# Optimization experiments

Measured on AMD Instinct MI355X. Metric: run time of the kernel, lower is better.

The kernel has to match this reference:

```python
import jax, jax.numpy as jnp
import numpy as np

B, S, D = 2, 2048, 1024
H, DH = 16, 64
EPS = 1e-5

def setup_inputs() -> dict:
    key = jax.random.key(0)
    ks = jax.random.split(key, 8)
    s = 0.02
    return {
        "x": jax.random.normal(ks[0], (B, S, D), dtype=jnp.float32),
        "ln_gamma": jnp.ones((D,), jnp.float32),
        "ln_beta": jnp.zeros((D,), jnp.float32),
        "wq": jax.random.normal(ks[1], (D, H * DH), jnp.float32) * s,
        "bq": jnp.zeros((H * DH,), jnp.float32),
        "wk": jax.random.normal(ks[2], (D, H * DH), jnp.float32) * s,
        "bk": jnp.zeros((H * DH,), jnp.float32),
        "wv": jax.random.normal(ks[3], (D, H * DH), jnp.float32) * s,
        "bv": jnp.zeros((H * DH,), jnp.float32),
        "wo": jax.random.normal(ks[4], (H * DH, D), jnp.float32) * s,
        "bo": jnp.zeros((D,), jnp.float32),
    }

def reference(x, ln_gamma, ln_beta, wq, bq, wk, bk, wv, bv, wo, bo):
    # Pre-LayerNorm over d_model
    mu = jnp.mean(x, axis=-1, keepdims=True)
    var = jnp.var(x, axis=-1, keepdims=True)
    xn = (x - mu) * jax.lax.rsqrt(var + EPS) * ln_gamma + ln_beta

    b, s, _ = xn.shape
    q = (xn @ wq + bq).reshape(b, s, H, DH)
    k = (xn @ wk + bk).reshape(b, s, H, DH)
    v = (xn @ wv + bv).reshape(b, s, H, DH)

    scale = jnp.sqrt(jnp.float32(DH))
    scores = jnp.einsum('bihd,bjhd->bhij', q, k) / scale  # [b,h,s,s]
    att = jax.nn.softmax(scores, axis=-1)
    out = jnp.einsum('bhij,bjhd->bihd', att, v).reshape(b, s, H * DH)
    return out @ wo + bo
```

## Files before the change

kernel.cpp:

```cpp
#include <hip/hip_runtime.h>
#include <math.h>

#define SEQ   2048
#define DM    1024
#define NHEAD 16
#define HD    64
#define NTOK  4096
#define EPS   1e-5f
#define SCALE_C 0.18033688f

typedef __attribute__((ext_vector_type(8))) short v8s;
typedef __attribute__((ext_vector_type(4))) float v4f;
typedef unsigned short ushort_t;

#define GLOAD16(g, l) __builtin_amdgcn_global_load_lds( \
    (const __attribute__((address_space(1))) unsigned int*)(g), \
    (__attribute__((address_space(3))) unsigned int*)(l), 16, 0, 0)

__device__ __forceinline__ unsigned short f2bf(float f) {
  union { float f; unsigned u; } v; v.f = f;
  unsigned r = v.u + 0x7FFFu + ((v.u >> 16) & 1u);
  return (unsigned short)(r >> 16);
}

__device__ __forceinline__ unsigned pack2_bf16(float a, float b) {
  union { float f; unsigned u; } ua, ub;
  ua.f = a; ub.f = b;
  return __builtin_amdgcn_perm(ub.u + 0x8000u, ua.u + 0x8000u, 0x07060302u);
}

__global__ __launch_bounds__(256) void ln_kernel(
    const float* __restrict__ x, const float* __restrict__ g,
    const float* __restrict__ be, ushort_t* __restrict__ y) {
  const int row = blockIdx.x;
  const int t = threadIdx.x;
  const float4 v = ((const float4*)(x + (size_t)row * DM))[t];
  float s  = v.x + v.y + v.z + v.w;
  float ss = v.x*v.x + v.y*v.y + v.z*v.z + v.w*v.w;
  #pragma unroll
  for (int off = 32; off > 0; off >>= 1) {
    s  += __shfl_down(s,  off, 64);
    ss += __shfl_down(ss, off, 64);
  }
  __shared__ float red[8];
  __shared__ float mu_s, rs_s;
  const int wid = t >> 6, lane = t & 63;
  if (lane == 0) { red[wid] = s; red[4 + wid] = ss; }
  __syncthreads();
  if (t == 0) {
    const float S  = red[0] + red[1] + red[2] + red[3];
    const float SS = red[4] + red[5] + red[6] + red[7];
    const float mu  = S * (1.0f / DM);
    const float var = SS * (1.0f / DM) - mu * mu;
    mu_s = mu; rs_s = rsqrtf(var + EPS);
  }
  __syncthreads();
  const float mu = mu_s, r = rs_s;
  const float4 gv = ((const float4*)g)[t];
  const float4 bv = ((const float4*)be)[t];
  ushort4 o;
  o.x = f2bf((v.x - mu) * r * gv.x + bv.x);
  o.y = f2bf((v.y - mu) * r * gv.y + bv.y);
  o.z = f2bf((v.z - mu) * r * gv.z + bv.z);
  o.w = f2bf((v.w - mu) * r * gv.w + bv.w);
  *(ushort4*)(y + (size_t)row * DM + t * 4) = o;
}

__global__ __launch_bounds__(256) void wt_kernel(
    const float* __restrict__ w0, const float* __restrict__ w1,
    const float* __restrict__ w2, const float* __restrict__ w3,
    ushort_t* __restrict__ o0, ushort_t* __restrict__ o1,
    ushort_t* __restrict__ o2, ushort_t* __restrict__ o3) {
  const int z = blockIdx.z;
  const float* w = (z==0) ? w0 : (z==1) ? w1 : (z==2) ? w2 : w3;
  ushort_t* o    = (z==0) ? o0 : (z==1) ? o1 : (z==2) ? o2 : o3;
  __shared__ float tile[64][65];
  const int t = threadIdx.x;
  const int n0 = blockIdx.x * 64, k0 = blockIdx.y * 64;
  const int r = t >> 4, c4 = (t & 15) * 4;
  #pragma unroll
  for (int i = 0; i < 4; ++i) {
    const float4 v = *(const float4*)(w + (size_t)(k0 + r + i*16) * DM + n0 + c4);
    tile[r + i*16][c4 + 0] = v.x;
    tile[r + i*16][c4 + 1] = v.y;
    tile[r + i*16][c4 + 2] = v.z;
    tile[r + i*16][c4 + 3] = v.w;
  }
  __syncthreads();
  #pragma unroll
  for (int i = 0; i < 4; ++i) {
    const int n = r + i*16;
    ushort4 o4;
    o4.x = f2bf(tile[c4 + 0][n]);
    o4.y = f2bf(tile[c4 + 1][n]);
    o4.z = f2bf(tile[c4 + 2][n]);
    o4.w = f2bf(tile[c4 + 3][n]);
    *(ushort4*)(o + (size_t)(n0 + n) * DM + k0 + c4) = o4;
  }
}

__device__ __forceinline__ void gemm_main(ushort_t* lsa, ushort_t* lsb,
    const ushort_t* A, const ushort_t* WT, int m0, int n0, v4f acc[4][4]) {
  const int tid = threadIdx.x;
  const int wid = tid >> 6, lane = tid & 63;
  const int mh = (wid & 1) << 6, nh = (wid >> 1) << 6;
  const int r16 = lane & 15, quad = lane >> 4;
  const int srow = lane >> 2, sch = lane & 3;
  for (int k0 = 0; k0 < DM; k0 += 32) {
    __syncthreads();
    #pragma unroll
    for (int j = 0; j < 2; ++j) {
      const int o = wid * 2 + j;
      GLOAD16(A  + (size_t)(m0 + o*16 + srow) * DM + k0 + sch*8, lsa + o*512);
      GLOAD16(WT + (size_t)(n0 + o*16 + srow) * DM + k0 + sch*8, lsb + o*512);
    }
    __syncthreads();
    v8s af[4], bfr[4];
    #pragma unroll
    for (int i = 0; i < 4; ++i) {
      af[i]  = *(const v8s*)(lsa + (mh + i*16 + r16)*32 + quad*8);
      bfr[i] = *(const v8s*)(lsb + (nh + i*16 + r16)*32 + quad*8);
    }
    #pragma unroll
    for (int i = 0; i < 4; ++i)
      #pragma unroll
      for (int j = 0; j < 4; ++j)
        acc[i][j] = __builtin_amdgcn_mfma_f32_16x16x32_bf16(af[i], bfr[j], acc[i][j], 0, 0, 0);
  }
}

__global__ __launch_bounds__(256, 2) void gemm_qkv(const ushort_t* __restrict__ xn,
    const ushort_t* __restrict__ wtq, const ushort_t* __restrict__ wtk, const ushort_t* __restrict__ wtv,
    const float* __restrict__ bq, const float* __restrict__ bk, const float* __restrict__ bv,
    ushort_t* __restrict__ qo, ushort_t* __restrict__ ko, ushort_t* __restrict__ vto) {
  __shared__ ushort_t lsa[128*32];
  __shared__ ushort_t lsb[128*32];
  const int z = blockIdx.z;
  const ushort_t* WT = (z == 0) ? wtq : (z == 1) ? wtk : wtv;
  const float* bias  = (z == 0) ? bq  : (z == 1) ? bk  : bv;
  const int m0 = blockIdx.y * 128, n0 = blockIdx.x * 128;
  v4f acc[4][4];
  #pragma unroll
  for (int i = 0; i < 4; ++i)
    #pragma unroll
    for (int j = 0; j < 4; ++j) acc[i][j] = (v4f){0.f, 0.f, 0.f, 0.f};
  gemm_main(lsa, lsb, xn, WT, m0, n0, acc);
  const int tid = threadIdx.x, wid = tid >> 6, lane = tid & 63;
  const int mh = (wid & 1) << 6, nh = (wid >> 1) << 6;
  const int r16 = lane & 15, quad = lane >> 4;
  if (z < 2) {
    ushort_t* out = (z == 0) ? qo : ko;
    const float sc = (z == 0) ? SCALE_C : 1.0f;
    #pragma unroll
    for (int bn = 0; bn < 4; ++bn) {
      const int col = n0 + nh + bn*16 + r16;
      const float bb = bias[col];
      #pragma unroll
      for (int am = 0; am < 4; ++am) {
        const int tb = m0 + mh + am*16 + quad*4;
        #pragma unroll
        for (int r = 0; r < 4; ++r)
          out[(size_t)(tb + r) * DM + col] = f2bf((acc[am][bn][r] + bb) * sc);
      }
    }
  } else {
    #pragma unroll
    for (int bn = 0; bn < 4; ++bn) {
      const int col = n0 + nh + bn*16 + r16;
      const float bb = bias[col];
      const int h = col >> 6, d = col & 63;
      #pragma unroll
      for (int am = 0; am < 4; ++am) {
        const int tb = m0 + mh + am*16 + quad*4;
        const int b = tb >> 11, t = tb & 2047;
        ushort4 o4;
        o4.x = f2bf(acc[am][bn][0] + bb);
        o4.y = f2bf(acc[am][bn][1] + bb);
        o4.z = f2bf(acc[am][bn][2] + bb);
        o4.w = f2bf(acc[am][bn][3] + bb);
        *(ushort4*)(vto + ((size_t)(b*NHEAD + h) * HD + d) * SEQ + t) = o4;
      }
    }
  }
}

__global__ __launch_bounds__(256, 2) void gemm_out(const ushort_t* __restrict__ A,
    const ushort_t* __restrict__ WT, const float* __restrict__ bias,
    float* __restrict__ out) {
  __shared__ ushort_t lsa[128*32];
  __shared__ ushort_t lsb[128*32];
  const int m0 = blockIdx.y * 128, n0 = blockIdx.x * 128;
  v4f acc[4][4];
  #pragma unroll
  for (int i = 0; i < 4; ++i)
    #pragma unroll
    for (int j = 0; j < 4; ++j) acc[i][j] = (v4f){0.f, 0.f, 0.f, 0.f};
  gemm_main(lsa, lsb, A, WT, m0, n0, acc);
  const int tid = threadIdx.x, wid = tid >> 6, lane = tid & 63;
  const int mh = (wid & 1) << 6, nh = (wid >> 1) << 6;
  const int r16 = lane & 15, quad = lane >> 4;
  #pragma unroll
  for (int bn = 0; bn < 4; ++bn) {
    const int col = n0 + nh + bn*16 + r16;
    const float bb = bias[col];
    #pragma unroll
    for (int am = 0; am < 4; ++am) {
      const int tb = m0 + mh + am*16 + quad*4;
      #pragma unroll
      for (int r = 0; r < 4; ++r)
        out[(size_t)(tb + r) * DM + col] = acc[am][bn][r] + bb;
    }
  }
}

#define PROW 72
__global__ __launch_bounds__(256, 4) void attn_kernel(
    const ushort_t* __restrict__ Q, const ushort_t* __restrict__ K,
    const ushort_t* __restrict__ Vt, ushort_t* __restrict__ O) {
  __shared__ ushort_t kbuf[8*512];
  __shared__ ushort_t vbuf[8*512];
  __shared__ ushort_t ptb[4*16*PROW];
  const int tid = threadIdx.x, wid = tid >> 6, lane = tid & 63;
  const int r16 = lane & 15, quad = lane >> 4;
  const int q0 = blockIdx.x * 64, bh = blockIdx.y;
  const int b = bh >> 4, h = bh & 15;
  const ushort_t* gQ = Q + (size_t)b * SEQ * DM + h * HD;
  const ushort_t* gK = K + (size_t)b * SEQ * DM + h * HD;
  const ushort_t* gV = Vt + (size_t)bh * HD * SEQ;

  const int qtok = q0 + wid * 16 + r16;
  const v8s qf0 = *(const v8s*)(gQ + (size_t)qtok * DM + quad * 8);
  const v8s qf1 = *(const v8s*)(gQ + (size_t)qtok * DM + 32 + quad * 8);
  v4f acco[4];
  #pragma unroll
  for (int i = 0; i < 4; ++i) acco[i] = (v4f){0.f, 0.f, 0.f, 0.f};
  float lrun = 0.f;
  ushort_t* ptw = ptb + wid * 16 * PROW;

  for (int kt = 0; kt < SEQ / 64; ++kt) {
    const int k0 = kt * 64;
    __syncthreads();
    if (wid < 2) {
      #pragma unroll
      for (int j = 0; j < 4; ++j) {
        const int o = (wid & 1) * 4 + j;
        GLOAD16(gK + (size_t)(k0 + (o >> 1) * 16 + r16) * DM + (o & 1) * 32 + quad * 8,
                kbuf + o * 512);
      }
    } else {
      #pragma unroll
      for (int j = 0; j < 4; ++j) {
        const int o = (wid & 1) * 4 + j;
        GLOAD16(gV + (size_t)((o & 3) * 16 + r16) * SEQ + k0 + (o >> 2) * 32 + quad * 8,
                vbuf + o * 512);
      }
    }
    __syncthreads();

    v4f sacc[4];
    #pragma unroll
    for (int g = 0; g < 4; ++g) sacc[g] = (v4f){0.f, 0.f, 0.f, 0.f};
    #pragma unroll
    for (int g = 0; g < 4; ++g) {
      const v8s ka0 = *(const v8s*)(kbuf + (g*2 + 0) * 512 + lane * 8);
      const v8s ka1 = *(const v8s*)(kbuf + (g*2 + 1) * 512 + lane * 8);
      sacc[g] = __builtin_amdgcn_mfma_f32_16x16x32_bf16(ka0, qf0, sacc[g], 0, 0, 0);
      sacc[g] = __builtin_amdgcn_mfma_f32_16x16x32_bf16(ka1, qf1, sacc[g], 0, 0, 0);
    }

    float ls = 0.f;
    #pragma unroll
    for (int g = 0; g < 4; ++g)
      #pragma unroll
      for (int r = 0; r < 4; ++r) {
        const float e = __builtin_amdgcn_exp2f(sacc[g][r]);
        sacc[g][r] = e;
        ls += e;
      }
    ls += __shfl_xor(ls, 16, 64);
    ls += __shfl_xor(ls, 32, 64);
    lrun += ls;

    #pragma unroll
    for (int g = 0; g < 4; ++g) {
      uint2 d2;
      d2.x = pack2_bf16(sacc[g][0], sacc[g][1]);
      d2.y = pack2_bf16(sacc[g][2], sacc[g][3]);
      *(uint2*)(ptw + r16 * PROW + g*16 + quad*4) = d2;
    }

    #pragma unroll
    for (int kb = 0; kb < 2; ++kb) {
      const v8s pb = *(const v8s*)(ptw + r16 * PROW + kb*32 + quad*8);
      #pragma unroll
      for (int dg = 0; dg < 4; ++dg) {
        const v8s vf = *(const v8s*)(vbuf + (kb*4 + dg) * 512 + lane * 8);
        acco[dg] = __builtin_amdgcn_mfma_f32_16x16x32_bf16(vf, pb, acco[dg], 0, 0, 0);
      }
    }
  }

  const float inv = 1.f / lrun;
  ushort_t* gO = O + (size_t)b * SEQ * DM + h * HD;
  #pragma unroll
  for (int dg = 0; dg < 4; ++dg) {
    ushort4 o4;
    o4.x = f2bf(acco[dg][0] * inv);
    o4.y = f2bf(acco[dg][1] * inv);
    o4.z = f2bf(acco[dg][2] * inv);
    o4.w = f2bf(acco[dg][3] * inv);
    *(ushort4*)(gO + (size_t)qtok * DM + dg*16 + quad*4) = o4;
  }
}

extern "C" void kernel_launch(void* const* d_in, const int* in_sizes, int n_in,
                              void* d_out, int out_size, void* d_ws, size_t ws_size,
                              hipStream_t stream) {
  const float* x     = (const float*)d_in[0];
  const float* gamma = (const float*)d_in[1];
  const float* beta  = (const float*)d_in[2];
  const float* wq    = (const float*)d_in[3];
  const float* bq    = (const float*)d_in[4];
  const float* wk    = (const float*)d_in[5];
  const float* bk    = (const float*)d_in[6];
  const float* wv    = (const float*)d_in[7];
  const float* bv    = (const float*)d_in[8];
  const float* wo    = (const float*)d_in[9];
  const float* bo    = (const float*)d_in[10];
  float* out = (float*)d_out;

  unsigned char* w8 = (unsigned char*)d_ws;
  const size_t MB = 1024 * 1024;
  ushort_t* xn  = (ushort_t*)(w8 + 0 * MB);
  ushort_t* qb  = (ushort_t*)(w8 + 8 * MB);
  ushort_t* kb  = (ushort_t*)(w8 + 16 * MB);
  ushort_t* vt  = (ushort_t*)(w8 + 24 * MB);
  ushort_t* wtq = (ushort_t*)(w8 + 32 * MB);
  ushort_t* wtk = (ushort_t*)(w8 + 34 * MB);
  ushort_t* wtv = (ushort_t*)(w8 + 36 * MB);
  ushort_t* wto = (ushort_t*)(w8 + 38 * MB);
  ushort_t* ob  = xn;

  ln_kernel<<<dim3(NTOK), dim3(256), 0, stream>>>(x, gamma, beta, xn);
  wt_kernel<<<dim3(16, 16, 4), dim3(256), 0, stream>>>(wq, wk, wv, wo, wtq, wtk, wtv, wto);
  gemm_qkv<<<dim3(8, 32, 3), dim3(256), 0, stream>>>(xn, wtq, wtk, wtv, bq, bk, bv, qb, kb, vt);
  attn_kernel<<<dim3(SEQ / 64, 2 * NHEAD), dim3(256), 0, stream>>>(qb, kb, vt, ob);
  gemm_out<<<dim3(8, 32, 1), dim3(256), 0, stream>>>(ob, wto, bo, out);
}
```

Baseline: 214.6 us.

## Repartition attention work by key/dim per wave and shrink output GEMM tiles

The attention kernel now has each wave own a 16-key slice of the tile for all 64 queries, writing P into a shared block buffer, and a 16-wide head-dim slice for the PV product. Row sums are reduced across waves through shared memory at the end. This lets each wave load only its own K and V fragments, at the cost of an extra block barrier per key tile. Separately, the output projection switches to its own 128x64 tile loop with twice as many blocks, trading per-block reuse for more parallelism in a small GEMM.

```diff
diff --git a/kernel.cpp b/kernel.cpp
--- a/kernel.cpp
+++ b/kernel.cpp
@@ -188,19 +188,43 @@
     const ushort_t* __restrict__ WT, const float* __restrict__ bias,
     float* __restrict__ out) {
   __shared__ ushort_t lsa[128*32];
-  __shared__ ushort_t lsb[128*32];
-  const int m0 = blockIdx.y * 128, n0 = blockIdx.x * 128;
-  v4f acc[4][4];
+  __shared__ ushort_t lsb[64*32];
+  const int tid = threadIdx.x, wid = tid >> 6, lane = tid & 63;
+  const int mh = (wid & 1) * 64, nh = (wid >> 1) * 32;
+  const int r16 = lane & 15, quad = lane >> 4;
+  const int srow = lane >> 2, sch = lane & 3;
+  const int m0 = blockIdx.y * 128, n0 = blockIdx.x * 64;
+  v4f acc[4][2];
   #pragma unroll
   for (int i = 0; i < 4; ++i)
     #pragma unroll
-    for (int j = 0; j < 4; ++j) acc[i][j] = (v4f){0.f, 0.f, 0.f, 0.f};
-  gemm_main(lsa, lsb, A, WT, m0, n0, acc);
-  const int tid = threadIdx.x, wid = tid >> 6, lane = tid & 63;
-  const int mh = (wid & 1) << 6, nh = (wid >> 1) << 6;
-  const int r16 = lane & 15, quad = lane >> 4;
-  #pragma unroll
-  for (int bn = 0; bn < 4; ++bn) {
+    for (int j = 0; j < 2; ++j) acc[i][j] = (v4f){0.f, 0.f, 0.f, 0.f};
+  for (int k0 = 0; k0 < DM; k0 += 32) {
+    __syncthreads();
+    #pragma unroll
+    for (int j = 0; j < 3; ++j) {
+      const int o = wid * 3 + j;
+      if (o < 8)
+        GLOAD16(A  + (size_t)(m0 + o*16 + srow) * DM + k0 + sch*8, lsa + o*512);
+      else
+        GLOAD16(WT + (size_t)(n0 + (o-8)*16 + srow) * DM + k0 + sch*8, lsb + (o-8)*512);
+    }
+    __syncthreads();
+    v8s af[4], bfr[2];
+    #pragma unroll
+    for (int i = 0; i < 4; ++i)
+      af[i] = *(const v8s*)(lsa + (mh + i*16 + r16)*32 + quad*8);
+    #pragma unroll
+    for (int j = 0; j < 2; ++j)
+      bfr[j] = *(const v8s*)(lsb + (nh + j*16 + r16)*32 + quad*8);
+    #pragma unroll
+    for (int i = 0; i < 4; ++i)
+      #pragma unroll
+      for (int j = 0; j < 2; ++j)
+        acc[i][j] = __builtin_amdgcn_mfma_f32_16x16x32_bf16(af[i], bfr[j], acc[i][j], 0, 0, 0);
+  }
+  #pragma unroll
+  for (int bn = 0; bn < 2; ++bn) {
     const int col = n0 + nh + bn*16 + r16;
     const float bb = bias[col];
     #pragma unroll
@@ -219,7 +243,8 @@
     const ushort_t* __restrict__ Vt, ushort_t* __restrict__ O) {
   __shared__ ushort_t kbuf[8*512];
   __shared__ ushort_t vbuf[8*512];
-  __shared__ ushort_t ptb[4*16*PROW];
+  __shared__ ushort_t pbuf[64*PROW];
+  __shared__ float    lred[4][64];
   const int tid = threadIdx.x, wid = tid >> 6, lane = tid & 63;
   const int r16 = lane & 15, quad = lane >> 4;
   const int q0 = blockIdx.x * 64, bh = blockIdx.y;
@@ -228,14 +253,17 @@
   const ushort_t* gK = K + (size_t)b * SEQ * DM + h * HD;
   const ushort_t* gV = Vt + (size_t)bh * HD * SEQ;
 
-  const int qtok = q0 + wid * 16 + r16;
-  const v8s qf0 = *(const v8s*)(gQ + (size_t)qtok * DM + quad * 8);
-  const v8s qf1 = *(const v8s*)(gQ + (size_t)qtok * DM + 32 + quad * 8);
+  v8s qfr[4][2];
+  #pragma unroll
+  for (int qa = 0; qa < 4; ++qa) {
+    const ushort_t* p = gQ + (size_t)(q0 + qa*16 + r16) * DM + quad * 8;
+    qfr[qa][0] = *(const v8s*)p;
+    qfr[qa][1] = *(const v8s*)(p + 32);
+  }
   v4f acco[4];
   #pragma unroll
   for (int i = 0; i < 4; ++i) acco[i] = (v4f){0.f, 0.f, 0.f, 0.f};
-  float lrun = 0.f;
-  ushort_t* ptw = ptb + wid * 16 * PROW;
+  float lrun[4] = {0.f, 0.f, 0.f, 0.f};
 
   for (int kt = 0; kt < SEQ / 64; ++kt) {
     const int k0 = kt * 64;
@@ -257,59 +285,61 @@
     }
     __syncthreads();
 
+    const v8s ka0 = *(const v8s*)(kbuf + (wid*2 + 0) * 512 + lane * 8);
+    const v8s ka1 = *(const v8s*)(kbuf + (wid*2 + 1) * 512 + lane * 8);
     v4f sacc[4];
     #pragma unroll
-    for (int g = 0; g < 4; ++g) sacc[g] = (v4f){0.f, 0.f, 0.f, 0.f};
-    #pragma unroll
-    for (int g = 0; g < 4; ++g) {
-      const v8s ka0 = *(const v8s*)(kbuf + (g*2 + 0) * 512 + lane * 8);
-      const v8s ka1 = *(const v8s*)(kbuf + (g*2 + 1) * 512 + lane * 8);
-      sacc[g] = __builtin_amdgcn_mfma_f32_16x16x32_bf16(ka0, qf0, sacc[g], 0, 0, 0);
-      sacc[g] = __builtin_amdgcn_mfma_f32_16x16x32_bf16(ka1, qf1, sacc[g], 0, 0, 0);
-    }
-
-    float ls = 0.f;
-    #pragma unroll
-    for (int g = 0; g < 4; ++g)
-      #pragma unroll
-      for (int r = 0; r < 4; ++r) {
-        const float e = __builtin_amdgcn_exp2f(sacc[g][r]);
-        sacc[g][r] = e;
-        ls += e;
-      }
-    ls += __shfl_xor(ls, 16, 64);
-    ls += __shfl_xor(ls, 32, 64);
-    lrun += ls;
-
-    #pragma unroll
-    for (int g = 0; g < 4; ++g) {
+    for (int qa = 0; qa < 4; ++qa) {
+      sacc[qa] = (v4f){0.f, 0.f, 0.f, 0.f};
+      sacc[qa] = __builtin_amdgcn_mfma_f32_16x16x32_bf16(ka0, qfr[qa][0], sacc[qa], 0, 0, 0);
+      sacc[qa] = __builtin_amdgcn_mfma_f32_16x16x32_bf16(ka1, qfr[qa][1], sacc[qa], 0, 0, 0);
+    }
+
+    #pragma unroll
+    for (int qa = 0; qa < 4; ++qa) {
+      const float e0 = __builtin_amdgcn_exp2f(sacc[qa][0]);
+      const float e1 = __builtin_amdgcn_exp2f(sacc[qa][1]);
+      const float e2 = __builtin_amdgcn_exp2f(sacc[qa][2]);
+      const float e3 = __builtin_amdgcn_exp2f(sacc[qa][3]);
+      float ls = (e0 + e1) + (e2 + e3);
+      ls += __shfl_xor(ls, 16, 64);
+      ls += __shfl_xor(ls, 32, 64);
+      lrun[qa] += ls;
       uint2 d2;
-      d2.x = pack2_bf16(sacc[g][0], sacc[g][1]);
-      d2.y = pack2_bf16(sacc[g][2], sacc[g][3]);
-      *(uint2*)(ptw + r16 * PROW + g*16 + quad*4) = d2;
-    }
-
-    #pragma unroll
-    for (int kb = 0; kb < 2; ++kb) {
-      const v8s pb = *(const v8s*)(ptw + r16 * PROW + kb*32 + quad*8);
-      #pragma unroll
-      for (int dg = 0; dg < 4; ++dg) {
-        const v8s vf = *(const v8s*)(vbuf + (kb*4 + dg) * 512 + lane * 8);
-        acco[dg] = __builtin_amdgcn_mfma_f32_16x16x32_bf16(vf, pb, acco[dg], 0, 0, 0);
-      }
-    }
-  }
-
-  const float inv = 1.f / lrun;
+      d2.x = pack2_bf16(e0, e1);
+      d2.y = pack2_bf16(e2, e3);
+      *(uint2*)(pbuf + (qa*16 + r16) * PROW + wid*16 + quad*4) = d2;
+    }
+
+    __syncthreads();
+
+    const v8s vf0 = *(const v8s*)(vbuf + (0*4 + wid) * 512 + lane * 8);
+    const v8s vf1 = *(const v8s*)(vbuf + (1*4 + wid) * 512 + lane * 8);
+    #pragma unroll
+    for (int qa = 0; qa < 4; ++qa) {
+      const v8s pb0 = *(const v8s*)(pbuf + (qa*16 + r16) * PROW + quad*8);
+      const v8s pb1 = *(const v8s*)(pbuf + (qa*16 + r16) * PROW + 32 + quad*8);
+      acco[qa] = __builtin_amdgcn_mfma_f32_16x16x32_bf16(vf0, pb0, acco[qa], 0, 0, 0);
+      acco[qa] = __builtin_amdgcn_mfma_f32_16x16x32_bf16(vf1, pb1, acco[qa], 0, 0, 0);
+    }
+  }
+
+  if (quad == 0) {
+    #pragma unroll
+    for (int qa = 0; qa < 4; ++qa) lred[wid][qa*16 + r16] = lrun[qa];
+  }
+  __syncthreads();
   ushort_t* gO = O + (size_t)b * SEQ * DM + h * HD;
   #pragma unroll
-  for (int dg = 0; dg < 4; ++dg) {
+  for (int qa = 0; qa < 4; ++qa) {
+    const int q = qa*16 + r16;
+    const float inv = 1.f / (((lred[0][q] + lred[1][q]) + (lred[2][q] + lred[3][q])));
     ushort4 o4;
-    o4.x = f2bf(acco[dg][0] * inv);
-    o4.y = f2bf(acco[dg][1] * inv);
-    o4.z = f2bf(acco[dg][2] * inv);
-    o4.w = f2bf(acco[dg][3] * inv);
-    *(ushort4*)(gO + (size_t)qtok * DM + dg*16 + quad*4) = o4;
+    o4.x = f2bf(acco[qa][0] * inv);
+    o4.y = f2bf(acco[qa][1] * inv);
+    o4.z = f2bf(acco[qa][2] * inv);
+    o4.w = f2bf(acco[qa][3] * inv);
+    *(ushort4*)(gO + (size_t)(q0 + q) * DM + wid*16 + quad*4) = o4;
   }
 }
 
@@ -345,5 +375,5 @@
   wt_kernel<<<dim3(16, 16, 4), dim3(256), 0, stream>>>(wq, wk, wv, wo, wtq, wtk, wtv, wto);
   gemm_qkv<<<dim3(8, 32, 3), dim3(256), 0, stream>>>(xn, wtq, wtk, wtv, bq, bk, bv, qb, kb, vt);
   attn_kernel<<<dim3(SEQ / 64, 2 * NHEAD), dim3(256), 0, stream>>>(qb, kb, vt, ob);
-  gemm_out<<<dim3(8, 32, 1), dim3(256), 0, stream>>>(ob, wto, bo, out);
-}
+  gemm_out<<<dim3(16, 32), dim3(256), 0, stream>>>(ob, wto, bo, out);
+}
```

Result: slower. 222.6 us (+3.7%).
